# Kernel optimization log

Measured on AMD Instinct MI355X. Metric: run time of the kernel, lower is better.

## Reference

```python
import jax, jax.numpy as jnp
import numpy as np

N = 50000   # nodes
E = 600000  # edges
D = 128     # node_input_dim
H = 128     # hidden_dim
A = 200000  # number of valid actions


def setup_inputs() -> dict:
    key = jax.random.key(0)
    ks = jax.random.split(key, 8)
    x = jax.random.normal(ks[0], (N, D), dtype=jnp.float32)
    edge_index = jax.random.randint(ks[1], (2, E), 0, N, dtype=jnp.int64)
    valid_actions = jax.random.randint(ks[2], (A, 2), 0, N, dtype=jnp.int64)
    # GCNConv uses glorot-style init for weight, zeros/uniform for bias; exact init is irrelevant for correctness
    s1 = 1.0 / np.sqrt(D)
    sH = 1.0 / np.sqrt(H)
    s2 = 1.0 / np.sqrt(2 * H)
    W1 = jax.random.uniform(ks[3], (D, H), jnp.float32, -s1, s1)
    b1 = jax.random.uniform(ks[4], (H,), jnp.float32, -s1, s1)
    W2 = jax.random.uniform(ks[5], (H, H), jnp.float32, -sH, sH)
    b2 = jax.random.uniform(ks[6], (H,), jnp.float32, -sH, sH)
    Wq = jax.random.uniform(ks[7], (2 * H, 1), jnp.float32, -s2, s2)
    bq = jnp.zeros((1,), jnp.float32)
    return {"x": x, "edge_index": edge_index, "valid_actions": valid_actions,
            "W1": W1, "b1": b1, "W2": W2, "b2": b2, "Wq": Wq, "bq": bq}


def _gcn_conv(h, src, dst, norm, W, b, n_nodes):
    # PyG GCNConv: x' = D^{-1/2} (A + I) D^{-1/2} X W + b
    h = h @ W                              # [N, H]
    msg = h[src] * norm[:, None]           # [E+N, H] gather + scale
    out = jax.ops.segment_sum(msg, dst, num_segments=n_nodes)  # scatter-add
    return out + b


def reference(x, edge_index, valid_actions, W1, b1, W2, b2, Wq, bq):
    n = x.shape[0]
    loops = jnp.arange(n, dtype=edge_index.dtype)
    src = jnp.concatenate([edge_index[0], loops])  # self-loops appended
    dst = jnp.concatenate([edge_index[1], loops])
    # symmetric normalization from in-degree of A+I (unit edge weights)
    deg = jax.ops.segment_sum(jnp.ones_like(dst, x.dtype), dst, num_segments=n)
    dis = jnp.where(deg > 0, jax.lax.rsqrt(deg), 0.0)
    norm = dis[src] * dis[dst]             # [E+N]

    h = jax.nn.relu(_gcn_conv(x, src, dst, norm, W1, b1, n))
    h = jax.nn.relu(_gcn_conv(h, src, dst, norm, W2, b2, n))

    # batched gather-concat-linear replacing the per-action Python loop
    pair = jnp.concatenate([h[valid_actions[:, 0]], h[valid_actions[:, 1]]], axis=-1)  # [A, 2H]
    q = pair @ Wq + bq                     # [A, 1]
    return q.reshape(-1)                   # torch.cat of A scalars -> [A]
```

## Files before the change

### kernel.cpp

```cpp
#include <hip/hip_runtime.h>
#include <hip/hip_bf16.h>

#define HDIM 128

typedef __attribute__((ext_vector_type(8))) short bf16x8_t;
typedef __attribute__((ext_vector_type(4))) float f32x4_t;

__device__ inline float bf16u_to_f(unsigned int u) { return __uint_as_float(u << 16); }
__device__ inline unsigned short bf16_rne(float x) {
    union { __hip_bfloat16 b; unsigned short u; } cv;
    cv.b = __float2bfloat16(x);
    return cv.u;
}
__device__ inline void split2(float x, unsigned short& h, unsigned short& l) {
    h = bf16_rne(x);
    l = bf16_rne(x - __uint_as_float((unsigned int)h << 16));
}

__global__ void deg_count_k(const int* __restrict__ dst, int* __restrict__ deg, int E) {
    int i = blockIdx.x * blockDim.x + threadIdx.x;
    if (i < E) atomicAdd(&deg[dst[i]], 1);
}

__global__ void scan_part_k(const int* __restrict__ deg, int* __restrict__ incl,
                            int* __restrict__ blocksum, int N) {
    __shared__ int s[256];
    const int tid = threadIdx.x;
    const int i = blockIdx.x * 256 + tid;
    int v = (i < N) ? deg[i] : 0;
    s[tid] = v;
    __syncthreads();
    #pragma unroll
    for (int off = 1; off < 256; off <<= 1) {
        int t = (tid >= off) ? s[tid - off] : 0;
        __syncthreads();
        s[tid] += t;
        __syncthreads();
    }
    if (i < N) incl[i] = s[tid];
    if (tid == 255) blocksum[blockIdx.x] = s[255];
}

__global__ void scan_block_k(int* __restrict__ blocksum, int NB) {
    __shared__ int s[256];
    const int tid = threadIdx.x;
    int v = (tid < NB) ? blocksum[tid] : 0;
    s[tid] = v;
    __syncthreads();
    #pragma unroll
    for (int off = 1; off < 256; off <<= 1) {
        int t = (tid >= off) ? s[tid - off] : 0;
        __syncthreads();
        s[tid] += t;
        __syncthreads();
    }
    if (tid < NB) blocksum[tid] = s[tid] - v;
}

__global__ void scan_final_k(const int* __restrict__ deg, const int* __restrict__ incl,
                             const int* __restrict__ blocksum, int* __restrict__ rowptr,
                             float* __restrict__ dis, int N, int E) {
    const int i = blockIdx.x * 256 + threadIdx.x;
    if (i < N) {
        rowptr[i] = blocksum[blockIdx.x] + incl[i] - deg[i];
        dis[i] = rsqrtf((float)deg[i] + 1.0f);
    }
    if (i == 0) rowptr[N] = E;
}

__global__ void fill_csr_k(const int* __restrict__ src, const int* __restrict__ dst,
                           const int* __restrict__ rowptr, int* __restrict__ cursor,
                           int* __restrict__ csr, int E) {
    int e = blockIdx.x * blockDim.x + threadIdx.x;
    if (e < E) {
        const int d = dst[e];
        const int pos = rowptr[d] + atomicAdd(&cursor[d], 1);
        csr[pos] = src[e];
    }
}

__global__ void pack_w_k(const float* __restrict__ W, unsigned short* __restrict__ hi,
                         unsigned short* __restrict__ lo) {
    const int idx = blockIdx.x * 256 + threadIdx.x;
    const int frag = idx >> 9;
    const int r = idx & 511;
    const int lane = r >> 3, j = r & 7;
    const int c = frag & 7, s = frag >> 3;
    const int col = (c << 4) | (lane & 15);
    const int k = (s << 5) + ((lane >> 4) << 3) + j;
    const float w = W[k * HDIM + col];
    unsigned short h, l;
    split2(w, h, l);
    hi[idx] = h;
    lo[idx] = l;
}

__global__ void prep_x_k(const float* __restrict__ X, unsigned short* __restrict__ hi,
                         unsigned short* __restrict__ lo, int total4) {
    int i = blockIdx.x * blockDim.x + threadIdx.x;
    if (i >= total4) return;
    const float4 v = reinterpret_cast<const float4*>(X)[i];
    ushort4 h, l;
    split2(v.x, h.x, l.x);
    split2(v.y, h.y, l.y);
    split2(v.z, h.z, l.z);
    split2(v.w, h.w, l.w);
    reinterpret_cast<ushort4*>(hi)[i] = h;
    reinterpret_cast<ushort4*>(lo)[i] = l;
}

__global__ __launch_bounds__(256) void mfma_gemm_k(
    const unsigned short* __restrict__ Xh, const unsigned short* __restrict__ Xl,
    const unsigned short* __restrict__ Wp, const float* __restrict__ dis,
    float* __restrict__ hs, int N) {
    __shared__ __align__(16) unsigned short wlds[32768];
    const int tid = threadIdx.x;
    {
        const float4* wsrc = reinterpret_cast<const float4*>(Wp);
        float4* wdst = reinterpret_cast<float4*>(wlds);
        #pragma unroll
        for (int i = 0; i < 16; ++i) wdst[tid + i * 256] = wsrc[tid + i * 256];
    }
    __syncthreads();

    const int wave = tid >> 6, lane = tid & 63;
    const int row0 = (blockIdx.x << 6) + (wave << 4);
    if (row0 >= N) return;
    const int lrow = lane & 15;
    const int kgrp = (lane >> 4) << 3;

    const long abase = ((long)(row0 + lrow) << 7) + kgrp;
    bf16x8_t ah[4], al[4];
    #pragma unroll
    for (int s = 0; s < 4; ++s) {
        ah[s] = *reinterpret_cast<const bf16x8_t*>(Xh + abase + (s << 5));
        al[s] = *reinterpret_cast<const bf16x8_t*>(Xl + abase + (s << 5));
    }

    f32x4_t acc[8];
    #pragma unroll
    for (int c = 0; c < 8; ++c) acc[c] = (f32x4_t){0.f, 0.f, 0.f, 0.f};

    #pragma unroll
    for (int s = 0; s < 4; ++s) {
        #pragma unroll
        for (int c = 0; c < 8; ++c) {
            const int fo = (((s << 3) + c) << 9) + (lane << 3);
            const bf16x8_t bh = *reinterpret_cast<const bf16x8_t*>(wlds + fo);
            const bf16x8_t bl = *reinterpret_cast<const bf16x8_t*>(wlds + 16384 + fo);
            acc[c] = __builtin_amdgcn_mfma_f32_16x16x32_bf16(ah[s], bh, acc[c], 0, 0, 0);
            acc[c] = __builtin_amdgcn_mfma_f32_16x16x32_bf16(al[s], bh, acc[c], 0, 0, 0);
            acc[c] = __builtin_amdgcn_mfma_f32_16x16x32_bf16(ah[s], bl, acc[c], 0, 0, 0);
        }
    }

    const int rbase = row0 + ((lane >> 4) << 2);
    float d[4];
    #pragma unroll
    for (int i = 0; i < 4; ++i) d[i] = dis[rbase + i];
    #pragma unroll
    for (int c = 0; c < 8; ++c) {
        const int col = (c << 4) | lrow;
        #pragma unroll
        for (int i = 0; i < 4; ++i)
            hs[((long)(rbase + i) << 7) + col] = acc[c][i] * d[i];
    }
}

__global__ __launch_bounds__(256) void gather_agg_k(
    const int* __restrict__ rowptr, const int* __restrict__ csr,
    const float* __restrict__ hs, const float* __restrict__ dis,
    const float* __restrict__ b, unsigned short* __restrict__ oh,
    unsigned short* __restrict__ ol, int N) {
    const int lane = threadIdx.x & 63;
    const int wid = (int)((blockIdx.x * (long)blockDim.x + threadIdx.x) >> 6);
    const int nw = (int)(((long)gridDim.x * blockDim.x) >> 6);
    const float2 bb = *reinterpret_cast<const float2*>(&b[lane * 2]);
    const int loff = lane * 2;
    for (int n = wid; n < N; n += nw) {
        const int r0 = rowptr[n], r1 = rowptr[n + 1];
        float2 acc = *reinterpret_cast<const float2*>(&hs[((long)n << 7) + loff]);
        float2 acc2 = {0.f, 0.f};
        int e = r0;
        for (; e + 4 <= r1; e += 4) {
            const int s0 = csr[e], s1 = csr[e + 1], s2 = csr[e + 2], s3 = csr[e + 3];
            const float2 v0 = *reinterpret_cast<const float2*>(&hs[((long)s0 << 7) + loff]);
            const float2 v1 = *reinterpret_cast<const float2*>(&hs[((long)s1 << 7) + loff]);
            const float2 v2 = *reinterpret_cast<const float2*>(&hs[((long)s2 << 7) + loff]);
            const float2 v3 = *reinterpret_cast<const float2*>(&hs[((long)s3 << 7) + loff]);
            acc.x += v0.x + v1.x;
            acc.y += v0.y + v1.y;
            acc2.x += v2.x + v3.x;
            acc2.y += v2.y + v3.y;
        }
        for (; e < r1; ++e) {
            const int s0 = csr[e];
            const float2 v0 = *reinterpret_cast<const float2*>(&hs[((long)s0 << 7) + loff]);
            acc.x += v0.x;
            acc.y += v0.y;
        }
        acc.x += acc2.x;
        acc.y += acc2.y;
        const float dv = dis[n];
        const float o0 = fmaxf(fmaf(acc.x, dv, bb.x), 0.f);
        const float o1 = fmaxf(fmaf(acc.y, dv, bb.y), 0.f);
        ushort2 h, l;
        split2(o0, h.x, l.x);
        split2(o1, h.y, l.y);
        *reinterpret_cast<ushort2*>(oh + ((long)n << 7) + loff) = h;
        *reinterpret_cast<ushort2*>(ol + ((long)n << 7) + loff) = l;
    }
}

__global__ __launch_bounds__(256) void proj_k(
    const unsigned short* __restrict__ hh, const unsigned short* __restrict__ hl,
    const float* __restrict__ Wq, float* __restrict__ pu, float* __restrict__ pv, int N) {
    const int lane = threadIdx.x & 63;
    const int wid = (int)((blockIdx.x * (long)blockDim.x + threadIdx.x) >> 6);
    const int nw = (int)(((long)gridDim.x * blockDim.x) >> 6);
    const float2 wu = *reinterpret_cast<const float2*>(&Wq[lane * 2]);
    const float2 wv = *reinterpret_cast<const float2*>(&Wq[HDIM + lane * 2]);
    for (int n = wid; n < N; n += nw) {
        const unsigned int ph = *reinterpret_cast<const unsigned int*>(hh + ((long)n << 7) + (lane << 1));
        const unsigned int pl = *reinterpret_cast<const unsigned int*>(hl + ((long)n << 7) + (lane << 1));
        const float h0 = bf16u_to_f(ph) + bf16u_to_f(pl);
        const float h1 = __uint_as_float(ph & 0xffff0000u) + __uint_as_float(pl & 0xffff0000u);
        float su = h0 * wu.x + h1 * wu.y;
        float sv = h0 * wv.x + h1 * wv.y;
        #pragma unroll
        for (int off = 32; off > 0; off >>= 1) {
            su += __shfl_down(su, off, 64);
            sv += __shfl_down(sv, off, 64);
        }
        if (lane == 0) {
            pu[n] = su;
            pv[n] = sv;
        }
    }
}

__global__ __launch_bounds__(256) void qhead_k(
    const float* __restrict__ pu, const float* __restrict__ pv,
    const int* __restrict__ va, const float* __restrict__ bq,
    float* __restrict__ out, int A) {
    const float bqv = bq[0];
    int i = blockIdx.x * blockDim.x + threadIdx.x;
    const int stride = gridDim.x * blockDim.x;
    for (; i < A; i += stride) {
        const int2 uv = reinterpret_cast<const int2*>(va)[i];
        out[i] = pu[uv.x] + pv[uv.y] + bqv;
    }
}

extern "C" void kernel_launch(void* const* d_in, const int* in_sizes, int n_in,
                              void* d_out, int out_size, void* d_ws, size_t ws_size,
                              hipStream_t stream) {
    const float* x   = (const float*)d_in[0];
    const int*   ei  = (const int*)d_in[1];
    const int*   va  = (const int*)d_in[2];
    const float* W1  = (const float*)d_in[3];
    const float* b1  = (const float*)d_in[4];
    const float* W2  = (const float*)d_in[5];
    const float* b2  = (const float*)d_in[6];
    const float* Wq  = (const float*)d_in[7];
    const float* bq  = (const float*)d_in[8];
    float* out = (float*)d_out;

    const int N = in_sizes[0] / HDIM;
    const int E = in_sizes[1] / 2;
    const int A = in_sizes[2] / 2;
    const int* esrc = ei;
    const int* edst = ei + E;

    char* p = (char*)d_ws;
    auto alloc = [&](size_t bytes) { char* r = p; p += (bytes + 255) & ~(size_t)255; return r; };
    int* deg_i    = (int*)alloc((size_t)N * 4);
    int* incl     = (int*)alloc((size_t)N * 4);
    int* rowptr   = (int*)alloc((size_t)(N + 1) * 4);
    int* cursor   = (int*)alloc((size_t)N * 4);
    int* blocksum = (int*)alloc(256 * 4);
    int* csr      = (int*)alloc((size_t)E * 4);
    float* dis    = (float*)alloc((size_t)N * 4);
    float* pu     = (float*)alloc((size_t)N * 4);
    float* pv     = (float*)alloc((size_t)N * 4);
    unsigned short* Wp1 = (unsigned short*)alloc(32768 * 2);
    unsigned short* Wp2 = (unsigned short*)alloc(32768 * 2);
    unsigned short* Xh  = (unsigned short*)alloc((size_t)N * HDIM * 2);
    unsigned short* Xl  = (unsigned short*)alloc((size_t)N * HDIM * 2);
    float* bufA   = (float*)alloc((size_t)N * HDIM * 4);

    const int T = 256;
    const int NB = (N + 255) / 256;

    hipMemsetAsync(deg_i, 0, (size_t)N * 4, stream);
    hipMemsetAsync(cursor, 0, (size_t)N * 4, stream);
    deg_count_k<<<(E + T - 1) / T, T, 0, stream>>>(edst, deg_i, E);
    scan_part_k<<<NB, 256, 0, stream>>>(deg_i, incl, blocksum, N);
    scan_block_k<<<1, 256, 0, stream>>>(blocksum, NB);
    scan_final_k<<<NB, 256, 0, stream>>>(deg_i, incl, blocksum, rowptr, dis, N, E);
    fill_csr_k<<<(E + T - 1) / T, T, 0, stream>>>(esrc, edst, rowptr, cursor, csr, E);

    pack_w_k<<<64, 256, 0, stream>>>(W1, Wp1, Wp1 + 16384);
    pack_w_k<<<64, 256, 0, stream>>>(W2, Wp2, Wp2 + 16384);
    prep_x_k<<<(N * HDIM / 4 + T - 1) / T, T, 0, stream>>>(x, Xh, Xl, N * HDIM / 4);

    mfma_gemm_k<<<(N + 63) / 64, 256, 0, stream>>>(Xh, Xl, Wp1, dis, bufA, N);
    gather_agg_k<<<2048, T, 0, stream>>>(rowptr, csr, bufA, dis, b1, Xh, Xl, N);

    mfma_gemm_k<<<(N + 63) / 64, 256, 0, stream>>>(Xh, Xl, Wp2, dis, bufA, N);
    gather_agg_k<<<2048, T, 0, stream>>>(rowptr, csr, bufA, dis, b2, Xh, Xl, N);

    proj_k<<<2048, T, 0, stream>>>(Xh, Xl, Wq, pu, pv, N);
    qhead_k<<<512, T, 0, stream>>>(pu, pv, va, bq, out, A);
}
```

Baseline: 297.1 us.

## Fuse CSR build into cooperative kernel, fold input split and projection into neighbors

```diff
diff --git a/kernel.cpp b/kernel.cpp
--- a/kernel.cpp
+++ b/kernel.cpp
@@ -1,5 +1,8 @@
 #include <hip/hip_runtime.h>
 #include <hip/hip_bf16.h>
+#include <hip/hip_cooperative_groups.h>
+
+namespace cg = cooperative_groups;
 
 #define HDIM 128
 
@@ -17,18 +20,25 @@
     l = bf16_rne(x - __uint_as_float((unsigned int)h << 16));
 }
 
-__global__ void deg_count_k(const int* __restrict__ dst, int* __restrict__ deg, int E) {
-    int i = blockIdx.x * blockDim.x + threadIdx.x;
-    if (i < E) atomicAdd(&deg[dst[i]], 1);
-}
-
-__global__ void scan_part_k(const int* __restrict__ deg, int* __restrict__ incl,
-                            int* __restrict__ blocksum, int N) {
+__global__ __launch_bounds__(256) void csr_build_k(
+    const int* __restrict__ src, const int* __restrict__ dst,
+    int* __restrict__ deg, int* __restrict__ cursor, int* __restrict__ incl,
+    int* __restrict__ blocksum, int* __restrict__ rowptr, int* __restrict__ csr,
+    float* __restrict__ dis, int N, int E) {
+    cg::grid_group grid = cg::this_grid();
+    const int tid = threadIdx.x, bid = blockIdx.x;
+    const int gid = bid * 256 + tid;
+    const int GSZ = 256 * 256;
     __shared__ int s[256];
-    const int tid = threadIdx.x;
-    const int i = blockIdx.x * 256 + tid;
-    int v = (i < N) ? deg[i] : 0;
-    s[tid] = v;
+
+    for (int i = gid; i < N; i += GSZ) { deg[i] = 0; cursor[i] = 0; }
+    grid.sync();
+
+    for (int e = gid; e < E; e += GSZ) atomicAdd(&deg[dst[e]], 1);
+    grid.sync();
+
+    const int myv = (gid < N) ? deg[gid] : 0;
+    s[tid] = myv;
     __syncthreads();
     #pragma unroll
     for (int off = 1; off < 256; off <<= 1) {
@@ -37,80 +47,61 @@
         s[tid] += t;
         __syncthreads();
     }
-    if (i < N) incl[i] = s[tid];
-    if (tid == 255) blocksum[blockIdx.x] = s[255];
-}
-
-__global__ void scan_block_k(int* __restrict__ blocksum, int NB) {
-    __shared__ int s[256];
-    const int tid = threadIdx.x;
-    int v = (tid < NB) ? blocksum[tid] : 0;
-    s[tid] = v;
-    __syncthreads();
-    #pragma unroll
-    for (int off = 1; off < 256; off <<= 1) {
-        int t = (tid >= off) ? s[tid - off] : 0;
+    if (gid < N) incl[gid] = s[tid];
+    if (tid == 255) blocksum[bid] = s[255];
+    grid.sync();
+
+    if (bid == 0) {
+        const int v2 = blocksum[tid];
         __syncthreads();
-        s[tid] += t;
+        s[tid] = v2;
         __syncthreads();
-    }
-    if (tid < NB) blocksum[tid] = s[tid] - v;
-}
-
-__global__ void scan_final_k(const int* __restrict__ deg, const int* __restrict__ incl,
-                             const int* __restrict__ blocksum, int* __restrict__ rowptr,
-                             float* __restrict__ dis, int N, int E) {
-    const int i = blockIdx.x * 256 + threadIdx.x;
-    if (i < N) {
-        rowptr[i] = blocksum[blockIdx.x] + incl[i] - deg[i];
-        dis[i] = rsqrtf((float)deg[i] + 1.0f);
-    }
-    if (i == 0) rowptr[N] = E;
-}
-
-__global__ void fill_csr_k(const int* __restrict__ src, const int* __restrict__ dst,
-                           const int* __restrict__ rowptr, int* __restrict__ cursor,
-                           int* __restrict__ csr, int E) {
-    int e = blockIdx.x * blockDim.x + threadIdx.x;
-    if (e < E) {
+        #pragma unroll
+        for (int off = 1; off < 256; off <<= 1) {
+            int t = (tid >= off) ? s[tid - off] : 0;
+            __syncthreads();
+            s[tid] += t;
+            __syncthreads();
+        }
+        blocksum[tid] = s[tid] - v2;
+    }
+    grid.sync();
+
+    if (gid < N) {
+        rowptr[gid] = blocksum[bid] + incl[gid] - deg[gid];
+        dis[gid] = rsqrtf((float)deg[gid] + 1.0f);
+    }
+    if (gid == 0) rowptr[N] = E;
+    grid.sync();
+
+    for (int e = gid; e < E; e += GSZ) {
         const int d = dst[e];
         const int pos = rowptr[d] + atomicAdd(&cursor[d], 1);
         csr[pos] = src[e];
     }
 }
 
-__global__ void pack_w_k(const float* __restrict__ W, unsigned short* __restrict__ hi,
-                         unsigned short* __restrict__ lo) {
+__global__ void pack_w2_k(const float* __restrict__ W1, const float* __restrict__ W2,
+                          unsigned short* __restrict__ Wp1, unsigned short* __restrict__ Wp2) {
     const int idx = blockIdx.x * 256 + threadIdx.x;
-    const int frag = idx >> 9;
-    const int r = idx & 511;
+    const float* W = (idx < 16384) ? W1 : W2;
+    unsigned short* hi = (idx < 16384) ? Wp1 : Wp2;
+    const int id = idx & 16383;
+    const int frag = id >> 9;
+    const int r = id & 511;
     const int lane = r >> 3, j = r & 7;
-    const int c = frag & 7, s = frag >> 3;
+    const int c = frag & 7, sfrag = frag >> 3;
     const int col = (c << 4) | (lane & 15);
-    const int k = (s << 5) + ((lane >> 4) << 3) + j;
-    const float w = W[k * HDIM + col];
+    const int k = (sfrag << 5) + ((lane >> 4) << 3) + j;
     unsigned short h, l;
-    split2(w, h, l);
-    hi[idx] = h;
-    lo[idx] = l;
-}
-
-__global__ void prep_x_k(const float* __restrict__ X, unsigned short* __restrict__ hi,
-                         unsigned short* __restrict__ lo, int total4) {
-    int i = blockIdx.x * blockDim.x + threadIdx.x;
-    if (i >= total4) return;
-    const float4 v = reinterpret_cast<const float4*>(X)[i];
-    ushort4 h, l;
-    split2(v.x, h.x, l.x);
-    split2(v.y, h.y, l.y);
-    split2(v.z, h.z, l.z);
-    split2(v.w, h.w, l.w);
-    reinterpret_cast<ushort4*>(hi)[i] = h;
-    reinterpret_cast<ushort4*>(lo)[i] = l;
-}
-
+    split2(W[k * HDIM + col], h, l);
+    hi[id] = h;
+    hi[id + 16384] = l;
+}
+
+template<bool FP32IN>
 __global__ __launch_bounds__(256) void mfma_gemm_k(
-    const unsigned short* __restrict__ Xh, const unsigned short* __restrict__ Xl,
+    const void* __restrict__ Xin, const unsigned short* __restrict__ Xl,
     const unsigned short* __restrict__ Wp, const float* __restrict__ dis,
     float* __restrict__ hs, int N) {
     __shared__ __align__(16) unsigned short wlds[32768];
@@ -131,10 +122,28 @@
 
     const long abase = ((long)(row0 + lrow) << 7) + kgrp;
     bf16x8_t ah[4], al[4];
-    #pragma unroll
-    for (int s = 0; s < 4; ++s) {
-        ah[s] = *reinterpret_cast<const bf16x8_t*>(Xh + abase + (s << 5));
-        al[s] = *reinterpret_cast<const bf16x8_t*>(Xl + abase + (s << 5));
+    if constexpr (FP32IN) {
+        const float* X = (const float*)Xin;
+        #pragma unroll
+        for (int s = 0; s < 4; ++s) {
+            const float4 a0 = *reinterpret_cast<const float4*>(X + abase + (s << 5));
+            const float4 a1 = *reinterpret_cast<const float4*>(X + abase + (s << 5) + 4);
+            float xv[8] = {a0.x, a0.y, a0.z, a0.w, a1.x, a1.y, a1.z, a1.w};
+            #pragma unroll
+            for (int j = 0; j < 8; ++j) {
+                unsigned short h, l;
+                split2(xv[j], h, l);
+                ah[s][j] = (short)h;
+                al[s][j] = (short)l;
+            }
+        }
+    } else {
+        const unsigned short* Xh = (const unsigned short*)Xin;
+        #pragma unroll
+        for (int s = 0; s < 4; ++s) {
+            ah[s] = *reinterpret_cast<const bf16x8_t*>(Xh + abase + (s << 5));
+            al[s] = *reinterpret_cast<const bf16x8_t*>(Xl + abase + (s << 5));
+        }
     }
 
     f32x4_t acc[8];
@@ -167,15 +176,22 @@
     }
 }
 
+template<bool PROJ>
 __global__ __launch_bounds__(256) void gather_agg_k(
     const int* __restrict__ rowptr, const int* __restrict__ csr,
     const float* __restrict__ hs, const float* __restrict__ dis,
     const float* __restrict__ b, unsigned short* __restrict__ oh,
-    unsigned short* __restrict__ ol, int N) {
+    unsigned short* __restrict__ ol, const float* __restrict__ Wq,
+    float* __restrict__ pu, float* __restrict__ pv, int N) {
     const int lane = threadIdx.x & 63;
     const int wid = (int)((blockIdx.x * (long)blockDim.x + threadIdx.x) >> 6);
     const int nw = (int)(((long)gridDim.x * blockDim.x) >> 6);
     const float2 bb = *reinterpret_cast<const float2*>(&b[lane * 2]);
+    float2 wu = {0.f, 0.f}, wv = {0.f, 0.f};
+    if constexpr (PROJ) {
+        wu = *reinterpret_cast<const float2*>(&Wq[lane * 2]);
+        wv = *reinterpret_cast<const float2*>(&Wq[HDIM + lane * 2]);
+    }
     const int loff = lane * 2;
     for (int n = wid; n < N; n += nw) {
         const int r0 = rowptr[n], r1 = rowptr[n + 1];
@@ -204,37 +220,24 @@
         const float dv = dis[n];
         const float o0 = fmaxf(fmaf(acc.x, dv, bb.x), 0.f);
         const float o1 = fmaxf(fmaf(acc.y, dv, bb.y), 0.f);
-        ushort2 h, l;
-        split2(o0, h.x, l.x);
-        split2(o1, h.y, l.y);
-        *reinterpret_cast<ushort2*>(oh + ((long)n << 7) + loff) = h;
-        *reinterpret_cast<ushort2*>(ol + ((long)n << 7) + loff) = l;
-    }
-}
-
-__global__ __launch_bounds__(256) void proj_k(
-    const unsigned short* __restrict__ hh, const unsigned short* __restrict__ hl,
-    const float* __restrict__ Wq, float* __restrict__ pu, float* __restrict__ pv, int N) {
-    const int lane = threadIdx.x & 63;
-    const int wid = (int)((blockIdx.x * (long)blockDim.x + threadIdx.x) >> 6);
-    const int nw = (int)(((long)gridDim.x * blockDim.x) >> 6);
-    const float2 wu = *reinterpret_cast<const float2*>(&Wq[lane * 2]);
-    const float2 wv = *reinterpret_cast<const float2*>(&Wq[HDIM + lane * 2]);
-    for (int n = wid; n < N; n += nw) {
-        const unsigned int ph = *reinterpret_cast<const unsigned int*>(hh + ((long)n << 7) + (lane << 1));
-        const unsigned int pl = *reinterpret_cast<const unsigned int*>(hl + ((long)n << 7) + (lane << 1));
-        const float h0 = bf16u_to_f(ph) + bf16u_to_f(pl);
-        const float h1 = __uint_as_float(ph & 0xffff0000u) + __uint_as_float(pl & 0xffff0000u);
-        float su = h0 * wu.x + h1 * wu.y;
-        float sv = h0 * wv.x + h1 * wv.y;
-        #pragma unroll
-        for (int off = 32; off > 0; off >>= 1) {
-            su += __shfl_down(su, off, 64);
-            sv += __shfl_down(sv, off, 64);
-        }
-        if (lane == 0) {
-            pu[n] = su;
-            pv[n] = sv;
+        if constexpr (!PROJ) {
+            ushort2 h, l;
+            split2(o0, h.x, l.x);
+            split2(o1, h.y, l.y);
+            *reinterpret_cast<ushort2*>(oh + ((long)n << 7) + loff) = h;
+            *reinterpret_cast<ushort2*>(ol + ((long)n << 7) + loff) = l;
+        } else {
+            float su = o0 * wu.x + o1 * wu.y;
+            float sv = o0 * wv.x + o1 * wv.y;
+            #pragma unroll
+            for (int off = 32; off > 0; off >>= 1) {
+                su += __shfl_down(su, off, 64);
+                sv += __shfl_down(sv, off, 64);
+            }
+            if (lane == 0) {
+                pu[n] = su;
+                pv[n] = sv;
+            }
         }
     }
 }
@@ -266,8 +269,8 @@
     const float* bq  = (const float*)d_in[8];
     float* out = (float*)d_out;
 
-    const int N = in_sizes[0] / HDIM;
-    const int E = in_sizes[1] / 2;
+    int N = in_sizes[0] / HDIM;
+    int E = in_sizes[1] / 2;
     const int A = in_sizes[2] / 2;
     const int* esrc = ei;
     const int* edst = ei + E;
@@ -290,26 +293,23 @@
     float* bufA   = (float*)alloc((size_t)N * HDIM * 4);
 
     const int T = 256;
-    const int NB = (N + 255) / 256;
-
-    hipMemsetAsync(deg_i, 0, (size_t)N * 4, stream);
-    hipMemsetAsync(cursor, 0, (size_t)N * 4, stream);
-    deg_count_k<<<(E + T - 1) / T, T, 0, stream>>>(edst, deg_i, E);
-    scan_part_k<<<NB, 256, 0, stream>>>(deg_i, incl, blocksum, N);
-    scan_block_k<<<1, 256, 0, stream>>>(blocksum, NB);
-    scan_final_k<<<NB, 256, 0, stream>>>(deg_i, incl, blocksum, rowptr, dis, N, E);
-    fill_csr_k<<<(E + T - 1) / T, T, 0, stream>>>(esrc, edst, rowptr, cursor, csr, E);
-
-    pack_w_k<<<64, 256, 0, stream>>>(W1, Wp1, Wp1 + 16384);
-    pack_w_k<<<64, 256, 0, stream>>>(W2, Wp2, Wp2 + 16384);
-    prep_x_k<<<(N * HDIM / 4 + T - 1) / T, T, 0, stream>>>(x, Xh, Xl, N * HDIM / 4);
-
-    mfma_gemm_k<<<(N + 63) / 64, 256, 0, stream>>>(Xh, Xl, Wp1, dis, bufA, N);
-    gather_agg_k<<<2048, T, 0, stream>>>(rowptr, csr, bufA, dis, b1, Xh, Xl, N);
-
-    mfma_gemm_k<<<(N + 63) / 64, 256, 0, stream>>>(Xh, Xl, Wp2, dis, bufA, N);
-    gather_agg_k<<<2048, T, 0, stream>>>(rowptr, csr, bufA, dis, b2, Xh, Xl, N);
-
-    proj_k<<<2048, T, 0, stream>>>(Xh, Xl, Wq, pu, pv, N);
+
+    {
+        void* args[] = {(void*)&esrc, (void*)&edst, (void*)&deg_i, (void*)&cursor,
+                        (void*)&incl, (void*)&blocksum, (void*)&rowptr, (void*)&csr,
+                        (void*)&dis, (void*)&N, (void*)&E};
+        hipLaunchCooperativeKernel((void*)csr_build_k, dim3(256), dim3(256), args, 0, stream);
+    }
+
+    pack_w2_k<<<128, 256, 0, stream>>>(W1, W2, Wp1, Wp2);
+
+    mfma_gemm_k<true><<<(N + 63) / 64, 256, 0, stream>>>(x, nullptr, Wp1, dis, bufA, N);
+    gather_agg_k<false><<<2048, T, 0, stream>>>(rowptr, csr, bufA, dis, b1,
+                                                Xh, Xl, nullptr, nullptr, nullptr, N);
+
+    mfma_gemm_k<false><<<(N + 63) / 64, 256, 0, stream>>>(Xh, Xl, Wp2, dis, bufA, N);
+    gather_agg_k<true><<<2048, T, 0, stream>>>(rowptr, csr, bufA, dis, b2,
+                                               nullptr, nullptr, Wq, pu, pv, N);
+
     qhead_k<<<512, T, 0, stream>>>(pu, pv, va, bq, out, A);
 }
```

After: 428.2 us. +44.1%, slower.
